# Optimization experiments

Measured on AMD Instinct MI355X. Metric: run time of the kernel, lower is better.

Reference implementation:

```python
import jax, jax.numpy as jnp
import numpy as np
import math

B, L, NV, PRED = 8, 512, 32, 96
D, PL, STRIDE = 128, 16, 8
E, TOPN, H = 8, 2, 512
P = (L - PL) // STRIDE + 2  # 64 patches (includes replication pad of STRIDE)
BAL_COEF, Z_COEF = 0.01, 0.001


def sinusoid_pe(n, d):
    pos = np.arange(n, dtype=np.float32)[:, None]
    div = np.exp(np.arange(0, d, 2, dtype=np.float32) * -(math.log(10000.0) / d))
    pe = np.zeros((n, d), dtype=np.float32)
    pe[:, 0::2] = np.sin(pos * div)
    pe[:, 1::2] = np.cos(pos * div)
    return jnp.asarray(pe)


def setup_inputs() -> dict:
    key = jax.random.key(0)
    ks = jax.random.split(key, 10)
    return {
        "x_enc": jax.random.normal(ks[0], (B, L, NV), jnp.float32),
        "x_mark_enc": jax.random.normal(ks[1], (B, L, 4), jnp.float32),
        "x_dec": jnp.zeros((B, 144, NV), jnp.float32),
        "x_mark_dec": jnp.zeros((B, 144, 4), jnp.float32),
        "W_patch": jax.random.normal(ks[2], (PL, D), jnp.float32) * 0.05,
        "Wg": jax.random.normal(ks[3], (D, E), jnp.float32) * 0.05,
        "W1": jax.random.normal(ks[4], (E, D, H), jnp.float32) * 0.05,
        "b1": jnp.zeros((E, H), jnp.float32),
        "W2": jax.random.normal(ks[5], (E, H, D), jnp.float32) * 0.05,
        "b2": jnp.zeros((E, D), jnp.float32),
        "W_head": jax.random.normal(ks[6], (D * P, PRED), jnp.float32) * 0.02,
        "b_head": jnp.zeros((PRED,), jnp.float32),
    }


def _forward(x_enc, W_patch, Wg, W1, b1, W2, b2, W_head, b_head):
    # instance norm over time (detached stats, like the torch code)
    means = jax.lax.stop_gradient(jnp.mean(x_enc, axis=1, keepdims=True))
    xc = x_enc - means
    stdev = jax.lax.stop_gradient(
        jnp.sqrt(jnp.mean((x_enc - means) ** 2, axis=1, keepdims=True) + 1e-5))
    xc = xc / stdev
    # [B, NV, L] -> replication pad right by STRIDE -> unfold into patches
    x = jnp.transpose(xc, (0, 2, 1))
    xp = jnp.pad(x, ((0, 0), (0, 0), (0, STRIDE)), mode="edge")
    idx = jnp.arange(P)[:, None] * STRIDE + jnp.arange(PL)[None, :]  # [P, PL]
    patches = xp[:, :, idx]  # [B, NV, P, PL]
    tok = patches.reshape(B * NV, P, PL)
    h = jnp.einsum("tpl,ld->tpd", tok, W_patch) + sinusoid_pe(P, D)[None]
    # ---- MoE over flattened tokens ----
    N = B * NV * P
    xf = h.reshape(N, D)
    logits = xf @ Wg                              # [N, E]
    probs = jax.nn.softmax(logits, axis=-1)
    gates, tops = jax.lax.top_k(probs, TOPN)      # [N, TOPN]
    # dense per-expert FFN (exact GELU, as nn.GELU default)
    eh = jax.nn.gelu(jnp.einsum("nd,edh->neh", xf, W1) + b1, approximate=False)
    eo = jnp.einsum("neh,ehd->ned", eh, W2) + b2  # [N, E, D]
    onehot = jax.nn.one_hot(tops, E, dtype=xf.dtype)          # [N, TOPN, E]
    cw = jnp.einsum("nk,nke->ne", gates, onehot)              # combine weights
    y = jnp.einsum("ne,ned->nd", cw, eo)
    # aux losses: load-balance + router z-loss
    mask = onehot.sum(axis=1)                                  # [N, E]
    balance = E * jnp.sum(jnp.mean(probs, axis=0) * jnp.mean(mask, axis=0)) / TOPN
    zloss = jnp.mean(jax.nn.logsumexp(logits, axis=-1) ** 2)
    aux = BAL_COEF * balance + Z_COEF * zloss
    # ---- head ----
    enc = y.reshape(B, NV, P, D).transpose(0, 1, 3, 2)         # [B, NV, D, P]
    flat = enc.reshape(B, NV, D * P)
    dec = flat @ W_head + b_head                               # [B, NV, PRED]
    dec = jnp.transpose(dec, (0, 2, 1))                        # [B, PRED, NV]
    dec = dec * stdev[:, 0, :][:, None, :] + means[:, 0, :][:, None, :]
    return dec, aux


def reference(x_enc, x_mark_enc, x_dec, x_mark_dec, W_patch, Wg, W1, b1, W2, b2,
              W_head, b_head):
    return _forward(x_enc, W_patch, Wg, W1, b1, W2, b2, W_head, b_head)
```

## Files before the change

### kernel.cpp

```cpp
#include <hip/hip_runtime.h>
#include <math.h>


typedef __attribute__((ext_vector_type(8))) short bf16x8;
typedef __attribute__((ext_vector_type(4))) float f32x4;

__device__ __forceinline__ float bf2f(unsigned short u){
  unsigned x = ((unsigned)u) << 16; float f; __builtin_memcpy(&f, &x, 4); return f;
}
__device__ __forceinline__ unsigned short f2bf(float f){
  unsigned x; __builtin_memcpy(&x, &f, 4);
  return (unsigned short)((x + 0x7FFFu + ((x >> 16) & 1u)) >> 16);
}
__device__ __forceinline__ float ldin(const void* p, int i, int f32){
  return f32 ? ((const float*)p)[i] : bf2f(((const unsigned short*)p)[i]);
}
__device__ __forceinline__ void stout(void* p, int i, float v, int f32){
  if (f32) ((float*)p)[i] = v; else ((unsigned short*)p)[i] = f2bf(v);
}
__device__ __forceinline__ f32x4 mfma16(bf16x8 a, bf16x8 b, f32x4 c){
  return __builtin_amdgcn_mfma_f32_16x16x32_bf16(a, b, c, 0, 0, 0);
}
#define BAR_RAW() asm volatile("s_waitcnt lgkmcnt(0)\n\ts_barrier" ::: "memory")
__device__ __forceinline__ float gelu_fast(float v){
  float u = v*v;
  float inner = v * fmaf(0.044715f, u, 1.0f);
  float e = __expf(-1.5957691216f * inner);
  return v / (1.0f + e);
}

#define OFF_SUMS   64
#define OFF_MEANS  256
#define OFF_STDS   1280
#define OFF_ECNT   2304
#define OFF_PE     3328
#define OFF_W1T    134400
#define OFF_W2T    1182976
#define OFF_WHT    2231552
#define OFF_CW     3804416
#define OFF_XFBF   4328704
#define OFF_FLATB  8523008
#define OFF_EO     12717312
#define OFF_TOKSLOT 79826176
#define OFF_DECP   79957248

__global__ __launch_bounds__(256) void k_prep_tr(const void* __restrict__ W1,
                                                 const void* __restrict__ W2,
                                                 const void* __restrict__ Wh,
                                                 int f32, float* pe,
                                                 unsigned short* W1T, unsigned short* W2T,
                                                 unsigned short* WhT){
  int t = threadIdx.x;
  if (blockIdx.x == 0){
    for (int i = t; i < 8192; i += 256){
      int p = i >> 7, d = i & 127;
      float freq = __expf(-(float)(d & ~1) * 0.07195578415606394f);
      float ang = (float)p * freq;
      pe[i] = (d & 1) ? __cosf(ang) : __sinf(ang);
    }
    return;
  }
  __shared__ float tile[32*33];
  int tb = blockIdx.x - 1;
  int r = t >> 3, cg = (t & 7) * 4;
  const void* src; unsigned short* dst;
  int in0, instride, out0, outstride;
  if (tb < 512){
    int e = tb >> 6, ti = tb & 63, d0 = (ti & 3) * 32, h0 = (ti >> 2) * 32;
    src = W1; dst = W1T;
    in0 = e*65536 + d0*512 + h0; instride = 512;
    out0 = e*65536 + h0*128 + d0; outstride = 128;
  } else if (tb < 1024){
    int tc = tb - 512;
    int e = tc >> 6, ti = tc & 63, d0 = (ti & 3) * 32, h0 = (ti >> 2) * 32;
    src = W2; dst = W2T;
    in0 = e*65536 + h0*128 + d0; instride = 128;
    out0 = e*65536 + d0*512 + h0; outstride = 512;
  } else {
    int tc = tb - 1024;
    int kt = tc / 3, nt = tc - kt*3;
    int k0 = kt*32, n0 = nt*32;
    src = Wh; dst = WhT;
    in0 = k0*96 + n0; instride = 96;
    out0 = n0*8192 + k0; outstride = 8192;
  }
  #pragma unroll
  for (int j = 0; j < 4; ++j)
    tile[r*33 + cg + j] = ldin(src, in0 + r*instride + cg + j, f32);
  __syncthreads();
  ushort4 o;
  o.x = f2bf(tile[(cg+0)*33 + r]);
  o.y = f2bf(tile[(cg+1)*33 + r]);
  o.z = f2bf(tile[(cg+2)*33 + r]);
  o.w = f2bf(tile[(cg+3)*33 + r]);
  *(ushort4*)(dst + out0 + r*outstride + cg) = o;
}

__global__ __launch_bounds__(256) void k_embed(const void* __restrict__ xe,
                                               const void* __restrict__ Wp,
                                               const void* __restrict__ Wg,
                                               int f32,
                                               const float* __restrict__ peg,
                                               float* means, float* stds,
                                               unsigned short* xfbf, float* cwg,
                                               float* sums,
                                               int* ecnt, int* elist, int* tokslot){
  __shared__ float xn[512];
  __shared__ float WpL[2048];
  __shared__ float WgL[1024];
  __shared__ float Xf[8192];
  __shared__ float lp[1024];
  __shared__ float taux[576];
  __shared__ float reds[256], redss[256];
  __shared__ float msh[2];
  __shared__ int lcnt[8], lbase[8];

  int bv = blockIdx.x;
  int b = bv >> 5, v = bv & 31;
  int t = threadIdx.x;

  if (t < 8) lcnt[t] = 0;

  float x0 = ldin(xe, (b*512 + t)*32 + v, f32);
  float x1 = ldin(xe, (b*512 + t + 256)*32 + v, f32);
  xn[t] = x0; xn[t+256] = x1;
  reds[t] = x0 + x1; redss[t] = x0*x0 + x1*x1;
  #pragma unroll
  for (int it = 0; it < 8; ++it)
    WpL[it*256 + t] = ldin(Wp, it*256 + t, f32);
  #pragma unroll
  for (int j = 0; j < 4; ++j)
    WgL[j*256 + t] = ldin(Wg, j*256 + t, f32);
  __syncthreads();
  for (int s = 128; s > 0; s >>= 1){
    if (t < s){ reds[t] += reds[t+s]; redss[t] += redss[t+s]; }
    __syncthreads();
  }
  if (t == 0){
    float m = reds[0] / 512.f;
    float sd = sqrtf(redss[0] / 512.f - m*m + 1e-5f);
    msh[0] = m; msh[1] = 1.f / sd;
    means[bv] = m; stds[bv] = sd;
  }
  __syncthreads();
  float mean = msh[0], rstd = msh[1];
  xn[t] = (xn[t] - mean) * rstd;
  xn[t+256] = (xn[t+256] - mean) * rstd;
  __syncthreads();
  {
    int p = t >> 2, q = t & 3;
    float tv[16];
    #pragma unroll
    for (int l = 0; l < 16; ++l){
      int xi = p*8 + l; if (xi > 511) xi = 511;
      tv[l] = xn[xi];
    }
    for (int dd = 0; dd < 32; ++dd){
      int d = q*32 + dd;
      float acc = peg[p*128 + d];
      #pragma unroll
      for (int l = 0; l < 16; ++l) acc += tv[l] * WpL[l*128 + d];
      Xf[p*128 + d] = acc;
    }
  }
  __syncthreads();
  if (t < 128){
    int p = t >> 1, half = t & 1;
    float s[8] = {0,0,0,0,0,0,0,0};
    for (int d = half*64; d < half*64 + 64; ++d){
      float xv = Xf[p*128 + d];
      #pragma unroll
      for (int e = 0; e < 8; ++e) s[e] += xv * WgL[d*8 + e];
    }
    #pragma unroll
    for (int e = 0; e < 8; ++e) lp[(p*2 + half)*8 + e] = s[e];
  }
  __syncthreads();
  int bi = 0, si = 0, lo0 = 0, lo1 = 0;
  if (t < 64){
    int p = t;
    float lg[8];
    #pragma unroll
    for (int e = 0; e < 8; ++e) lg[e] = lp[(p*2)*8 + e] + lp[(p*2+1)*8 + e];
    float m = lg[0];
    #pragma unroll
    for (int e = 1; e < 8; ++e) m = fmaxf(m, lg[e]);
    float pr[8]; float se = 0.f;
    #pragma unroll
    for (int e = 0; e < 8; ++e){ pr[e] = __expf(lg[e] - m); se += pr[e]; }
    float inv = 1.f / se;
    float lse = m + logf(se);
    #pragma unroll
    for (int e = 0; e < 8; ++e) pr[e] *= inv;
    float best = -1.f;
    #pragma unroll
    for (int e = 0; e < 8; ++e) if (pr[e] > best){ best = pr[e]; bi = e; }
    float sec = -1.f;
    #pragma unroll
    for (int e = 0; e < 8; ++e) if (e != bi && pr[e] > sec){ sec = pr[e]; si = e; }
    #pragma unroll
    for (int e = 0; e < 8; ++e){
      float w = (e == bi) ? best : ((e == si) ? sec : 0.f);
      cwg[(bv*64 + p)*8 + e] = w;
      taux[p*9 + e] = pr[e];
    }
    taux[p*9 + 8] = lse * lse;
    lp[p] = (float)bi; lp[64 + p] = (float)si;
    lo0 = atomicAdd(&lcnt[bi], 1);
    lo1 = atomicAdd(&lcnt[si], 1);
  }
  __syncthreads();
  if (t < 8) lbase[t] = atomicAdd(ecnt + t*32, lcnt[t]);
  __syncthreads();
  if (t < 64){
    int n = bv*64 + t;
    int p0 = lbase[bi] + lo0, p1 = lbase[si] + lo1;
    elist[bi*16384 + p0] = n;
    elist[si*16384 + p1] = n;
    tokslot[n*2]     = (bi << 14) + p0;
    tokslot[n*2 + 1] = (si << 14) + p1;
  }
  if (t < 17){
    float s = 0.f;
    if (t < 8){ for (int p = 0; p < 64; ++p) s += taux[p*9 + t]; }
    else if (t < 16){
      int e = t - 8;
      for (int p = 0; p < 64; ++p)
        s += ((int)lp[p] == e || (int)lp[64+p] == e) ? 1.f : 0.f;
    }
    else { for (int p = 0; p < 64; ++p) s += taux[p*9 + 8]; }
    atomicAdd(sums + t, s);
  }
  #pragma unroll
  for (int pass = 0; pass < 4; ++pass){
    int idx = pass*256 + t;
    int base = idx*8;
    bf16x8 o;
    #pragma unroll
    for (int j = 0; j < 8; ++j) o[j] = (short)f2bf(Xf[base + j]);
    *(bf16x8*)(xfbf + bv*8192 + base) = o;
  }
}

__global__ __launch_bounds__(256, 3) void k_moe(const unsigned short* __restrict__ xfbf,
                                                const unsigned short* __restrict__ W1T,
                                                const unsigned short* __restrict__ W2T,
                                                const void* __restrict__ b1g,
                                                int f32,
                                                const float* __restrict__ cwg,
                                                const int* __restrict__ ecnt,
                                                const int* __restrict__ elist,
                                                float* __restrict__ Eo){
  __shared__ __align__(16) short Ag[32*72];
  __shared__ float cws[32];
  __shared__ int   lsn[32];

  int t = threadIdx.x;
  int e = 8, ti = 0;
  {
    int acc = 0, bk = blockIdx.x;
    #pragma unroll
    for (int ee = 0; ee < 8; ++ee){
      int tl = (ecnt[ee*32] + 31) >> 5;
      if (e == 8 && bk < acc + tl){ e = ee; ti = bk - acc; }
      acc += tl;
    }
  }
  if (e == 8) return;
  int cntE = ecnt[e*32];
  int tbase = ti*32;

  int wave = t >> 6, lane = t & 63;
  int quad = lane >> 4, li = lane & 15;
  int c1 = wave * 16;
  int c2 = wave * 32;

  const unsigned short* W1e = W1T + e*65536;
  const unsigned short* W2e = W2T + e*65536;

  bf16x8 w1f[2][4];
  float biasv[2];
  #pragma unroll
  for (int ks = 0; ks < 4; ++ks)
    w1f[0][ks] = *(const bf16x8*)(W1e + (c1 + li)*128 + ks*32 + quad*8);
  biasv[0] = ldin(b1g, e*512 + c1 + li, f32);

  if (t < 32){
    int ok = (tbase + t) < cntE;
    int n = ok ? elist[e*16384 + tbase + t] : 0;
    lsn[t] = n;
    cws[t] = ok ? cwg[n*8 + e] : 0.f;
  }
  BAR_RAW();

  int n0 = lsn[li], n1 = lsn[16 + li];
  bf16x8 a0[4], a1[4];
  #pragma unroll
  for (int ks = 0; ks < 4; ++ks){
    int kk = ks*32 + quad*8;
    a0[ks] = *(const bf16x8*)(xfbf + n0*128 + kk);
    a1[ks] = *(const bf16x8*)(xfbf + n1*128 + kk);
  }
  float cwv[2][4];
  #pragma unroll
  for (int rt = 0; rt < 2; ++rt)
    #pragma unroll
    for (int r = 0; r < 4; ++r)
      cwv[rt][r] = cws[rt*16 + quad*4 + r];

  f32x4 Yacc[2][2];
  #pragma unroll
  for (int a = 0; a < 2; ++a)
    #pragma unroll
    for (int bb = 0; bb < 2; ++bb){ f32x4 z = {0.f,0.f,0.f,0.f}; Yacc[a][bb] = z; }

  #pragma unroll
  for (int hc = 0; hc < 8; ++hc){
    const int cur = hc & 1, nxt = cur ^ 1;
    bf16x8 w2f[2][2];
    #pragma unroll
    for (int ks = 0; ks < 2; ++ks)
      #pragma unroll
      for (int ct = 0; ct < 2; ++ct)
        w2f[ks][ct] = *(const bf16x8*)(W2e + (c2 + ct*16 + li)*512 + hc*64 + ks*32 + quad*8);
    if (hc < 7){
      #pragma unroll
      for (int ks = 0; ks < 4; ++ks)
        w1f[nxt][ks] = *(const bf16x8*)(W1e + ((hc+1)*64 + c1 + li)*128 + ks*32 + quad*8);
      biasv[nxt] = ldin(b1g, e*512 + (hc+1)*64 + c1 + li, f32);
    }
    f32x4 acc1a = {0.f,0.f,0.f,0.f}, acc1b = {0.f,0.f,0.f,0.f};
    #pragma unroll
    for (int ks = 0; ks < 4; ++ks){
      acc1a = mfma16(a0[ks], w1f[cur][ks], acc1a);
      acc1b = mfma16(a1[ks], w1f[cur][ks], acc1b);
    }
    BAR_RAW();
    {
      float bias = biasv[cur];
      #pragma unroll
      for (int r = 0; r < 4; ++r){
        float g0 = gelu_fast(acc1a[r] + bias);
        Ag[(quad*4 + r)*72 + c1 + li] = (short)f2bf(g0 * cwv[0][r]);
        float g1 = gelu_fast(acc1b[r] + bias);
        Ag[(16 + quad*4 + r)*72 + c1 + li] = (short)f2bf(g1 * cwv[1][r]);
      }
    }
    BAR_RAW();
    #pragma unroll
    for (int ks = 0; ks < 2; ++ks){
      int kk = ks*32 + quad*8;
      bf16x8 g0 = *(const bf16x8*)(Ag + li*72 + kk);
      bf16x8 g1 = *(const bf16x8*)(Ag + (16 + li)*72 + kk);
      Yacc[0][0] = mfma16(g0, w2f[ks][0], Yacc[0][0]);
      Yacc[0][1] = mfma16(g0, w2f[ks][1], Yacc[0][1]);
      Yacc[1][0] = mfma16(g1, w2f[ks][0], Yacc[1][0]);
      Yacc[1][1] = mfma16(g1, w2f[ks][1], Yacc[1][1]);
    }
  }
  #pragma unroll
  for (int ct = 0; ct < 2; ++ct){
    int col = c2 + ct*16 + li;
    #pragma unroll
    for (int rt = 0; rt < 2; ++rt)
      #pragma unroll
      for (int r = 0; r < 4; ++r){
        int row = rt*16 + quad*4 + r;
        if (tbase + row < cntE)
          Eo[(size_t)((e << 14) + tbase + row)*128 + col] = (rt ? ((f32x4*)0, Yacc[1][ct]) : Yacc[0][ct])[r];
      }
  }
}

__global__ __launch_bounds__(256) void k_flat(const float* __restrict__ Eo,
                                              const int* __restrict__ tokslot,
                                              const float* __restrict__ cwg,
                                              const void* __restrict__ b2g,
                                              int f32,
                                              unsigned short* __restrict__ flatb){
  __shared__ float Yl[64*130];
  __shared__ float b2f[1024];
  __shared__ float cwl[512];
  __shared__ int tsl[128];
  int bv = blockIdx.x;
  int t = threadIdx.x;
  if (t < 64){
    int2 v = *(const int2*)(tokslot + (bv*64 + t)*2);
    tsl[t*2] = v.x; tsl[t*2+1] = v.y;
  }
  #pragma unroll
  for (int j = 0; j < 4; ++j) b2f[j*256 + t] = ldin(b2g, j*256 + t, f32);
  #pragma unroll
  for (int j = 0; j < 2; ++j) cwl[j*256 + t] = cwg[bv*512 + j*256 + t];
  __syncthreads();
  #pragma unroll
  for (int pass = 0; pass < 32; ++pass){
    int idx = pass*256 + t;
    int row = idx >> 7, col = idx & 127;
    Yl[row*130 + col] = Eo[(size_t)tsl[row*2]*128 + col]
                      + Eo[(size_t)tsl[row*2+1]*128 + col];
  }
  __syncthreads();
  int d = t >> 1, ph = (t & 1) * 32;
  float b2c[8];
  #pragma unroll
  for (int e = 0; e < 8; ++e) b2c[e] = b2f[e*128 + d];
  unsigned short ob[32];
  for (int j = 0; j < 32; ++j){
    int p = ph + j;
    float add = 0.f;
    #pragma unroll
    for (int e = 0; e < 8; ++e) add += cwl[p*8 + e] * b2c[e];
    ob[j] = f2bf(Yl[p*130 + d] + add);
  }
  #pragma unroll
  for (int m = 0; m < 4; ++m)
    *(bf16x8*)(flatb + bv*8192 + d*64 + ph + m*8) = *(bf16x8*)(ob + m*8);
}

__global__ __launch_bounds__(256) void k_head(const unsigned short* __restrict__ flatb,
                                              const unsigned short* __restrict__ WhT,
                                              float* __restrict__ dec_part){
  int t = threadIdx.x;
  int mt = blockIdx.x & 15, kc = blockIdx.x >> 4;
  int wave = t >> 6, lane = t & 63, quad = lane >> 4, li = lane & 15;
  int kbase = kc*512 + wave*128;
  f32x4 acc[6];
  #pragma unroll
  for (int nt = 0; nt < 6; ++nt){ f32x4 z = {0.f,0.f,0.f,0.f}; acc[nt] = z; }
  #pragma unroll
  for (int ks = 0; ks < 4; ++ks){
    int k = kbase + ks*32 + quad*8;
    bf16x8 a = *(const bf16x8*)(flatb + (mt*16 + li)*8192 + k);
    #pragma unroll
    for (int nt = 0; nt < 6; ++nt){
      bf16x8 b = *(const bf16x8*)(WhT + (nt*16 + li)*8192 + k);
      acc[nt] = mfma16(a, b, acc[nt]);
    }
  }
  __shared__ float redsh[4][16][96];
  #pragma unroll
  for (int nt = 0; nt < 6; ++nt)
    #pragma unroll
    for (int r = 0; r < 4; ++r)
      redsh[wave][quad*4 + r][nt*16 + li] = acc[nt][r];
  __syncthreads();
  #pragma unroll
  for (int u = 0; u < 6; ++u){
    int o = t*6 + u;
    int row = o / 96, col = o % 96;
    float s = redsh[0][row][col] + redsh[1][row][col] + redsh[2][row][col] + redsh[3][row][col];
    dec_part[kc*24576 + (mt*16 + row)*96 + col] = s;
  }
}

__global__ __launch_bounds__(256) void k_final(const float* __restrict__ dec_part,
                                               const void* __restrict__ bh,
                                               int f32,
                                               const float* __restrict__ means,
                                               const float* __restrict__ stds,
                                               const float* __restrict__ sums,
                                               void* out){
  int o = blockIdx.x*256 + threadIdx.x;
  int b = o / 3072, rem = o % 3072, j = rem >> 5, v = rem & 31;
  int bv = b*32 + v;
  int idx = bv*96 + j;
  float s = 0.f;
  #pragma unroll
  for (int kc = 0; kc < 16; ++kc) s += dec_part[kc*24576 + idx];
  float val = (s + ldin(bh, j, f32)) * stds[bv] + means[bv];
  stout(out, o, val, f32);
  if (o == 0){
    float bal = 0.f;
    for (int e = 0; e < 8; ++e) bal += (sums[e] / 16384.f) * (sums[8+e] / 16384.f);
    bal = 8.f * bal / 2.f;
    float aux = 0.01f * bal + 0.001f * (sums[16] / 16384.f);
    stout(out, 24576, aux, f32);
  }
}

extern "C" void kernel_launch(void* const* d_in, const int* in_sizes, int n_in,
                              void* d_out, int out_size, void* d_ws, size_t ws_size,
                              hipStream_t stream){
  const void* xe = d_in[0];
  const void* Wp = d_in[4];
  const void* Wg = d_in[5];
  const void* W1 = d_in[6];
  const void* b1 = d_in[7];
  const void* W2 = d_in[8];
  const void* b2 = d_in[9];
  const void* Wh = d_in[10];
  const void* bh = d_in[11];

  int f32 = 1;
  if (in_sizes && n_in > 0 && in_sizes[0] == 262144) f32 = 0;

  char* ws = (char*)d_ws;
  float* sums  = (float*)(ws + OFF_SUMS);
  float* means = (float*)(ws + OFF_MEANS);
  float* stds  = (float*)(ws + OFF_STDS);
  int*   ecnt  = (int*)(ws + OFF_ECNT);
  float* pe    = (float*)(ws + OFF_PE);
  unsigned short* W1T   = (unsigned short*)(ws + OFF_W1T);
  unsigned short* W2T   = (unsigned short*)(ws + OFF_W2T);
  unsigned short* WhT   = (unsigned short*)(ws + OFF_WHT);
  float* cw    = (float*)(ws + OFF_CW);
  unsigned short* xfbf  = (unsigned short*)(ws + OFF_XFBF);
  unsigned short* flatb = (unsigned short*)(ws + OFF_FLATB);
  int*   elist = (int*)(ws + OFF_FLATB);
  float* Eo    = (float*)(ws + OFF_EO);
  int*   tokslot = (int*)(ws + OFF_TOKSLOT);
  float* dec_part = (float*)(ws + OFF_DECP);

  hipMemsetAsync(ws, 0, 3328, stream);
  k_prep_tr<<<1793, 256, 0, stream>>>(W1, W2, Wh, f32, pe, W1T, W2T, WhT);
  k_embed<<<256, 256, 0, stream>>>(xe, Wp, Wg, f32, pe, means, stds,
                                   xfbf, cw, sums, ecnt, elist, tokslot);
  k_moe<<<1032, 256, 0, stream>>>(xfbf, W1T, W2T, b1, f32, cw, ecnt, elist, Eo);
  k_flat<<<256, 256, 0, stream>>>(Eo, tokslot, cw, b2, f32, flatb);
  k_head<<<256, 256, 0, stream>>>(flatb, WhT, dec_part);
  k_final<<<96, 256, 0, stream>>>(dec_part, bh, f32, means, stds, sums, d_out);
}
```

Baseline: 163.9 us.

## Restructure MoE kernel with full-H LDS staging and persistent tile loop

The MoE kernel now stages each 32-token tile's gathered activations in LDS, computes the whole 512-wide hidden layer into a larger LDS buffer, and then runs the second GEMM in one pass. This removes the per-chunk barriers of the old 8-step H-chunk loop. Blocks loop over tiles with a grid of 768 instead of launching 1032 one-tile blocks. The positional encoding is computed inline in the embed kernel instead of in a separate prep block with a global round-trip. The 42KB of LDS per block may reduce occupancy, and W2 loads are no longer prefetched ahead of the MFMAs.

```diff
diff --git a/kernel.cpp b/kernel.cpp
--- a/kernel.cpp
+++ b/kernel.cpp
@@ -33,7 +33,6 @@
 #define OFF_MEANS  256
 #define OFF_STDS   1280
 #define OFF_ECNT   2304
-#define OFF_PE     3328
 #define OFF_W1T    134400
 #define OFF_W2T    1182976
 #define OFF_WHT    2231552
@@ -47,21 +46,12 @@
 __global__ __launch_bounds__(256) void k_prep_tr(const void* __restrict__ W1,
                                                  const void* __restrict__ W2,
                                                  const void* __restrict__ Wh,
-                                                 int f32, float* pe,
+                                                 int f32,
                                                  unsigned short* W1T, unsigned short* W2T,
                                                  unsigned short* WhT){
   int t = threadIdx.x;
-  if (blockIdx.x == 0){
-    for (int i = t; i < 8192; i += 256){
-      int p = i >> 7, d = i & 127;
-      float freq = __expf(-(float)(d & ~1) * 0.07195578415606394f);
-      float ang = (float)p * freq;
-      pe[i] = (d & 1) ? __cosf(ang) : __sinf(ang);
-    }
-    return;
-  }
   __shared__ float tile[32*33];
-  int tb = blockIdx.x - 1;
+  int tb = blockIdx.x;
   int r = t >> 3, cg = (t & 7) * 4;
   const void* src; unsigned short* dst;
   int in0, instride, out0, outstride;
@@ -100,7 +90,6 @@
                                                const void* __restrict__ Wp,
                                                const void* __restrict__ Wg,
                                                int f32,
-                                               const float* __restrict__ peg,
                                                float* means, float* stds,
                                                unsigned short* xfbf, float* cwg,
                                                float* sums,
@@ -157,7 +146,9 @@
     }
     for (int dd = 0; dd < 32; ++dd){
       int d = q*32 + dd;
-      float acc = peg[p*128 + d];
+      float freq = __expf(-(float)(d & ~1) * 0.07195578415606394f);
+      float ang = (float)p * freq;
+      float acc = (d & 1) ? __cosf(ang) : __sinf(ang);
       #pragma unroll
       for (int l = 0; l < 16; ++l) acc += tv[l] * WpL[l*128 + d];
       Xf[p*128 + d] = acc;
@@ -251,124 +242,133 @@
                                                 const int* __restrict__ ecnt,
                                                 const int* __restrict__ elist,
                                                 float* __restrict__ Eo){
-  __shared__ __align__(16) short Ag[32*72];
-  __shared__ float cws[32];
-  __shared__ int   lsn[32];
+  __shared__ __align__(16) char lds[42240];
+  short* Xs  = (short*)(lds);
+  short* Ag  = (short*)(lds + 8704);
+  float* cws = (float*)(lds + 41984);
+  int*   lsn = (int*)(lds + 42112);
 
   int t = threadIdx.x;
-  int e = 8, ti = 0;
-  {
-    int acc = 0, bk = blockIdx.x;
-    #pragma unroll
-    for (int ee = 0; ee < 8; ++ee){
-      int tl = (ecnt[ee*32] + 31) >> 5;
-      if (e == 8 && bk < acc + tl){ e = ee; ti = bk - acc; }
-      acc += tl;
-    }
-  }
-  if (e == 8) return;
-  int cntE = ecnt[e*32];
-  int tbase = ti*32;
-
   int wave = t >> 6, lane = t & 63;
   int quad = lane >> 4, li = lane & 15;
-  int c1 = wave * 16;
-  int c2 = wave * 32;
-
-  const unsigned short* W1e = W1T + e*65536;
-  const unsigned short* W2e = W2T + e*65536;
-
-  bf16x8 w1f[2][4];
-  float biasv[2];
-  #pragma unroll
-  for (int ks = 0; ks < 4; ++ks)
-    w1f[0][ks] = *(const bf16x8*)(W1e + (c1 + li)*128 + ks*32 + quad*8);
-  biasv[0] = ldin(b1g, e*512 + c1 + li, f32);
-
-  if (t < 32){
-    int ok = (tbase + t) < cntE;
-    int n = ok ? elist[e*16384 + tbase + t] : 0;
-    lsn[t] = n;
-    cws[t] = ok ? cwg[n*8 + e] : 0.f;
-  }
-  BAR_RAW();
-
-  int n0 = lsn[li], n1 = lsn[16 + li];
-  bf16x8 a0[4], a1[4];
-  #pragma unroll
-  for (int ks = 0; ks < 4; ++ks){
-    int kk = ks*32 + quad*8;
-    a0[ks] = *(const bf16x8*)(xfbf + n0*128 + kk);
-    a1[ks] = *(const bf16x8*)(xfbf + n1*128 + kk);
-  }
-  float cwv[2][4];
-  #pragma unroll
-  for (int rt = 0; rt < 2; ++rt)
-    #pragma unroll
-    for (int r = 0; r < 4; ++r)
-      cwv[rt][r] = cws[rt*16 + quad*4 + r];
-
-  f32x4 Yacc[2][2];
-  #pragma unroll
-  for (int a = 0; a < 2; ++a)
-    #pragma unroll
-    for (int bb = 0; bb < 2; ++bb){ f32x4 z = {0.f,0.f,0.f,0.f}; Yacc[a][bb] = z; }
-
-  #pragma unroll
-  for (int hc = 0; hc < 8; ++hc){
-    const int cur = hc & 1, nxt = cur ^ 1;
-    bf16x8 w2f[2][2];
-    #pragma unroll
-    for (int ks = 0; ks < 2; ++ks)
-      #pragma unroll
-      for (int ct = 0; ct < 2; ++ct)
-        w2f[ks][ct] = *(const bf16x8*)(W2e + (c2 + ct*16 + li)*512 + hc*64 + ks*32 + quad*8);
-    if (hc < 7){
-      #pragma unroll
-      for (int ks = 0; ks < 4; ++ks)
-        w1f[nxt][ks] = *(const bf16x8*)(W1e + ((hc+1)*64 + c1 + li)*128 + ks*32 + quad*8);
-      biasv[nxt] = ldin(b1g, e*512 + (hc+1)*64 + c1 + li, f32);
-    }
-    f32x4 acc1a = {0.f,0.f,0.f,0.f}, acc1b = {0.f,0.f,0.f,0.f};
+  int c1p = wave * 128;
+  int c2  = wave * 32;
+
+  for (int tb = blockIdx.x; tb < 1536; tb += 768){
+    int e = 8, ti = 0;
+    {
+      int acc = 0;
+      #pragma unroll
+      for (int ee = 0; ee < 8; ++ee){
+        int tl = (ecnt[ee*32] + 31) >> 5;
+        if (e == 8 && tb < acc + tl){ e = ee; ti = tb - acc; }
+        acc += tl;
+      }
+    }
+    if (e == 8) break;
+    int cntE = ecnt[e*32];
+    int tbase = ti*32;
+
+    const unsigned short* W1e = W1T + e*65536;
+    const unsigned short* W2e = W2T + e*65536;
+
+    bf16x8 w1p[4];
+    #pragma unroll
+    for (int ks = 0; ks < 4; ++ks)
+      w1p[ks] = *(const bf16x8*)(W1e + (c1p + li)*128 + ks*32 + quad*8);
+    float bias0 = ldin(b1g, e*512 + c1p + li, f32);
+
+    if (t < 32){
+      int ok = (tbase + t) < cntE;
+      int n = ok ? elist[e*16384 + tbase + t] : 0;
+      lsn[t] = n;
+      cws[t] = ok ? cwg[n*8 + e] : 0.f;
+    }
+    BAR_RAW();
+    #pragma unroll
+    for (int pass = 0; pass < 2; ++pass){
+      int idx = pass*256 + t;
+      int row = idx >> 4, kg = idx & 15;
+      int n = lsn[row];
+      *(bf16x8*)(Xs + row*136 + kg*8) =
+        *(const bf16x8*)(xfbf + n*128 + kg*8);
+    }
+    float cwv[2][4];
+    #pragma unroll
+    for (int rt = 0; rt < 2; ++rt)
+      #pragma unroll
+      for (int r = 0; r < 4; ++r)
+        cwv[rt][r] = cws[rt*16 + quad*4 + r];
+    BAR_RAW();
+
+    bf16x8 a0[4], a1[4];
     #pragma unroll
     for (int ks = 0; ks < 4; ++ks){
-      acc1a = mfma16(a0[ks], w1f[cur][ks], acc1a);
-      acc1b = mfma16(a1[ks], w1f[cur][ks], acc1b);
+      int kk = ks*32 + quad*8;
+      a0[ks] = *(const bf16x8*)(Xs + li*136 + kk);
+      a1[ks] = *(const bf16x8*)(Xs + (16 + li)*136 + kk);
+    }
+
+    #pragma unroll
+    for (int ct = 0; ct < 8; ++ct){
+      bf16x8 bw[4];
+      float bias;
+      if (ct == 0){
+        #pragma unroll
+        for (int ks = 0; ks < 4; ++ks) bw[ks] = w1p[ks];
+        bias = bias0;
+      } else {
+        #pragma unroll
+        for (int ks = 0; ks < 4; ++ks)
+          bw[ks] = *(const bf16x8*)(W1e + (c1p + ct*16 + li)*128 + ks*32 + quad*8);
+        bias = ldin(b1g, e*512 + c1p + ct*16 + li, f32);
+      }
+      f32x4 acc0 = {0.f,0.f,0.f,0.f}, acc1 = {0.f,0.f,0.f,0.f};
+      #pragma unroll
+      for (int ks = 0; ks < 4; ++ks){
+        acc0 = mfma16(a0[ks], bw[ks], acc0);
+        acc1 = mfma16(a1[ks], bw[ks], acc1);
+      }
+      int col = c1p + ct*16 + li;
+      #pragma unroll
+      for (int r = 0; r < 4; ++r){
+        float g0 = gelu_fast(acc0[r] + bias);
+        Ag[(quad*4 + r)*520 + col] = (short)f2bf(g0 * cwv[0][r]);
+        float g1 = gelu_fast(acc1[r] + bias);
+        Ag[(16 + quad*4 + r)*520 + col] = (short)f2bf(g1 * cwv[1][r]);
+      }
     }
     BAR_RAW();
-    {
-      float bias = biasv[cur];
-      #pragma unroll
-      for (int r = 0; r < 4; ++r){
-        float g0 = gelu_fast(acc1a[r] + bias);
-        Ag[(quad*4 + r)*72 + c1 + li] = (short)f2bf(g0 * cwv[0][r]);
-        float g1 = gelu_fast(acc1b[r] + bias);
-        Ag[(16 + quad*4 + r)*72 + c1 + li] = (short)f2bf(g1 * cwv[1][r]);
-      }
-    }
-    BAR_RAW();
-    #pragma unroll
-    for (int ks = 0; ks < 2; ++ks){
+
+    f32x4 Yacc[2][2];
+    #pragma unroll
+    for (int a = 0; a < 2; ++a)
+      #pragma unroll
+      for (int bb = 0; bb < 2; ++bb){ f32x4 z = {0.f,0.f,0.f,0.f}; Yacc[a][bb] = z; }
+    #pragma unroll
+    for (int ks = 0; ks < 16; ++ks){
       int kk = ks*32 + quad*8;
-      bf16x8 g0 = *(const bf16x8*)(Ag + li*72 + kk);
-      bf16x8 g1 = *(const bf16x8*)(Ag + (16 + li)*72 + kk);
-      Yacc[0][0] = mfma16(g0, w2f[ks][0], Yacc[0][0]);
-      Yacc[0][1] = mfma16(g0, w2f[ks][1], Yacc[0][1]);
-      Yacc[1][0] = mfma16(g1, w2f[ks][0], Yacc[1][0]);
-      Yacc[1][1] = mfma16(g1, w2f[ks][1], Yacc[1][1]);
-    }
-  }
-  #pragma unroll
-  for (int ct = 0; ct < 2; ++ct){
-    int col = c2 + ct*16 + li;
-    #pragma unroll
-    for (int rt = 0; rt < 2; ++rt)
-      #pragma unroll
-      for (int r = 0; r < 4; ++r){
-        int row = rt*16 + quad*4 + r;
-        if (tbase + row < cntE)
-          Eo[(size_t)((e << 14) + tbase + row)*128 + col] = (rt ? ((f32x4*)0, Yacc[1][ct]) : Yacc[0][ct])[r];
-      }
+      bf16x8 g0 = *(const bf16x8*)(Ag + li*520 + kk);
+      bf16x8 g1 = *(const bf16x8*)(Ag + (16 + li)*520 + kk);
+      bf16x8 b0 = *(const bf16x8*)(W2e + (c2 + li)*512 + kk);
+      bf16x8 b1 = *(const bf16x8*)(W2e + (c2 + 16 + li)*512 + kk);
+      Yacc[0][0] = mfma16(g0, b0, Yacc[0][0]);
+      Yacc[0][1] = mfma16(g0, b1, Yacc[0][1]);
+      Yacc[1][0] = mfma16(g1, b0, Yacc[1][0]);
+      Yacc[1][1] = mfma16(g1, b1, Yacc[1][1]);
+    }
+    #pragma unroll
+    for (int ct = 0; ct < 2; ++ct){
+      int col = c2 + ct*16 + li;
+      #pragma unroll
+      for (int rt = 0; rt < 2; ++rt)
+        #pragma unroll
+        for (int r = 0; r < 4; ++r){
+          int row = rt*16 + quad*4 + r;
+          if (tbase + row < cntE)
+            Eo[(size_t)((e << 14) + tbase + row)*128 + col] = Yacc[rt][ct][r];
+        }
+    }
   }
 }
 
@@ -500,7 +500,6 @@
   float* means = (float*)(ws + OFF_MEANS);
   float* stds  = (float*)(ws + OFF_STDS);
   int*   ecnt  = (int*)(ws + OFF_ECNT);
-  float* pe    = (float*)(ws + OFF_PE);
   unsigned short* W1T   = (unsigned short*)(ws + OFF_W1T);
   unsigned short* W2T   = (unsigned short*)(ws + OFF_W2T);
   unsigned short* WhT   = (unsigned short*)(ws + OFF_WHT);
@@ -513,10 +512,10 @@
   float* dec_part = (float*)(ws + OFF_DECP);
 
   hipMemsetAsync(ws, 0, 3328, stream);
-  k_prep_tr<<<1793, 256, 0, stream>>>(W1, W2, Wh, f32, pe, W1T, W2T, WhT);
-  k_embed<<<256, 256, 0, stream>>>(xe, Wp, Wg, f32, pe, means, stds,
+  k_prep_tr<<<1792, 256, 0, stream>>>(W1, W2, Wh, f32, W1T, W2T, WhT);
+  k_embed<<<256, 256, 0, stream>>>(xe, Wp, Wg, f32, means, stds,
                                    xfbf, cw, sums, ecnt, elist, tokslot);
-  k_moe<<<1032, 256, 0, stream>>>(xfbf, W1T, W2T, b1, f32, cw, ecnt, elist, Eo);
+  k_moe<<<768, 256, 0, stream>>>(xfbf, W1T, W2T, b1, f32, cw, ecnt, elist, Eo);
   k_flat<<<256, 256, 0, stream>>>(Eo, tokslot, cw, b2, f32, flatb);
   k_head<<<256, 256, 0, stream>>>(flatb, WhT, dec_part);
   k_final<<<96, 256, 0, stream>>>(dec_part, bh, f32, means, stds, sums, d_out);
```

Measured after the change: 170.2 us. 1.04x slower.
